# Kernel tuning notes

Hardware: AMD Instinct MI355X
Metric: run time of the kernel (lower is better)

## Reference

```python
import jax, jax.numpy as jnp
import numpy as np
import math

B, S, D, H, DH, R = 2, 2048, 1024, 16, 64, 8
EPS = 1e-5


def setup_inputs() -> dict:
    key = jax.random.key(0)
    ks = jax.random.split(key, 8)
    hidden_states = jax.random.normal(ks[0], (B, S, D), jnp.float32)
    # causal boolean mask (batch, seq, seq); every row has >=1 valid entry
    causal = jnp.tril(jnp.ones((S, S), dtype=bool))
    attention_mask = jnp.broadcast_to(causal, (B, S, S))
    # lora: (n_layers=1, 4, batch, hidden, rank); [0]=qA,[1]=kA,[2]=qB,[3]=kB
    lora = jax.random.normal(ks[1], (1, 4, B, D, R), jnp.float32) * 0.02
    ln_w = jnp.ones((D,), jnp.float32)
    Wq = jax.random.normal(ks[2], (D, D), jnp.float32) * 0.02
    Wk = jax.random.normal(ks[3], (D, D), jnp.float32) * 0.02
    Wv = jax.random.normal(ks[4], (D, D), jnp.float32) * 0.02
    Wo = jax.random.normal(ks[5], (D, D), jnp.float32) * 0.02
    return dict(hidden_states=hidden_states, attention_mask=attention_mask,
                lora=lora, ln_w=ln_w, Wq=Wq, Wk=Wk, Wv=Wv, Wo=Wo)


def _rms_ln(x, w):
    # model_center LayerNorm with bias=False == RMS layernorm
    var = jnp.mean(x * x, axis=-1, keepdims=True)
    return x * jax.lax.rsqrt(var + EPS) * w


def _lora_delta(h, A, Bm):
    # h: (b,s,D), A: (b,D,R), Bm: (b,R,D);  h + (h@A)@Bm * 2
    z = jnp.einsum('bsd,bdr->bsr', h, A)
    return h + jnp.einsum('bsr,brd->bsd', z, Bm) * 2


def reference(hidden_states, attention_mask, lora, ln_w, Wq, Wk, Wv, Wo):
    b, s, _ = hidden_states.shape
    x = _rms_ln(hidden_states, ln_w)
    h_q = x @ Wq.T
    h_k = x @ Wk.T
    h_v = x @ Wv.T
    layer = lora[0]  # (4, b, D, R)
    h_q = _lora_delta(h_q, layer[0], jnp.swapaxes(layer[2], 1, 2))
    h_k = _lora_delta(h_k, layer[1], jnp.swapaxes(layer[3], 1, 2))
    q = h_q.reshape(b, s, H, DH)
    k = h_k.reshape(b, s, H, DH)
    v = h_v.reshape(b, s, H, DH)
    score = jnp.einsum('bqhd,bkhd->bhqk', q, k) / math.sqrt(DH)
    m = attention_mask[:, None, :, :]  # (b,1,s,s)
    score = jnp.where(m, score, -jnp.inf)
    p = jax.nn.softmax(score, axis=-1)
    p = jnp.where(m, p, jnp.float32(0))
    out = jnp.einsum('bhqk,bkhd->bqhd', p, v).reshape(b, s, H * DH)
    out = out @ Wo.T
    return hidden_states + out
```

## Files before the change

kernel.cpp:

```cpp
#include <hip/hip_runtime.h>

typedef __bf16 bf16;
typedef __bf16 bf16x4 __attribute__((ext_vector_type(4)));
typedef __bf16 bf16x8 __attribute__((ext_vector_type(8)));
typedef float f32x4 __attribute__((ext_vector_type(4)));

#define DM 1024
#define NROW 4096
#define SEQ 2048
#define HDIM 64
#define NEGBIG -30000.0f

#define SWB(base, row, bcol) \
  ((char*)(base) + (row) * 128 + ((bcol) ^ (((row) & 7) << 4)))

__device__ __forceinline__ void async16(const bf16* g, bf16* l) {
  __builtin_amdgcn_global_load_lds(
      (const __attribute__((address_space(1))) unsigned int*)g,
      (__attribute__((address_space(3))) unsigned int*)l, 16, 0, 0);
}

template <bool F32OUT>
__device__ __forceinline__ void gemm128(const bf16* __restrict__ A,
                                        const bf16* __restrict__ Bw,
                                        bf16* __restrict__ Cb,
                                        float* __restrict__ Cf,
                                        const float* __restrict__ resid,
                                        int m0, int n0) {
  __shared__ __align__(16) bf16 sA[2][128 * 32];
  __shared__ __align__(16) bf16 sB[2][128 * 32];
  const int t = threadIdx.x;
  const int lane = t & 63;
  const int w = t >> 6;
  const int wm = (w & 1) * 64;
  const int wn = (w >> 1) * 64;
  const int lr = lane & 15;
  const int kg = lane >> 4;

  f32x4 acc[4][4];
#pragma unroll
  for (int i = 0; i < 4; i++)
#pragma unroll
    for (int j = 0; j < 4; j++)
#pragma unroll
      for (int r = 0; r < 4; r++) acc[i][j][r] = 0.0f;

  const int srow = t >> 2;
  const int scol = (t & 3) * 8;
  const bf16* gA = A + (size_t)(m0 + srow) * DM + scol;
  const bf16* gB = Bw + (size_t)(n0 + srow) * DM + scol;

#define GSTAGE(k0_, buf_)                                \
  {                                                      \
    async16(gA + (k0_), &sA[buf_][t * 8]);               \
    async16(gA + (k0_) + 64 * DM, &sA[buf_][t * 8 + 2048]); \
    async16(gB + (k0_), &sB[buf_][t * 8]);               \
    async16(gB + (k0_) + 64 * DM, &sB[buf_][t * 8 + 2048]); \
  }

  GSTAGE(0, 0);
  __syncthreads();

  for (int k0 = 0; k0 < DM; k0 += 32) {
    const int cur = (k0 >> 5) & 1;
    if (k0 + 32 < DM) GSTAGE(k0 + 32, cur ^ 1);
    bf16x8 av[4], bv[4];
#pragma unroll
    for (int mi = 0; mi < 4; mi++)
      av[mi] = *(const bf16x8*)&sA[cur][(wm + mi * 16 + lr) * 32 + kg * 8];
#pragma unroll
    for (int nj = 0; nj < 4; nj++)
      bv[nj] = *(const bf16x8*)&sB[cur][(wn + nj * 16 + lr) * 32 + kg * 8];
    __builtin_amdgcn_s_setprio(1);
#pragma unroll
    for (int mi = 0; mi < 4; mi++)
#pragma unroll
      for (int nj = 0; nj < 4; nj++)
        acc[mi][nj] = __builtin_amdgcn_mfma_f32_16x16x32_bf16(av[mi], bv[nj],
                                                              acc[mi][nj], 0, 0, 0);
    __builtin_amdgcn_s_setprio(0);
    __syncthreads();
  }
#undef GSTAGE

#pragma unroll
  for (int mi = 0; mi < 4; mi++) {
#pragma unroll
    for (int r = 0; r < 4; r++) {
      const int grow = m0 + wm + mi * 16 + kg * 4 + r;
      const size_t base = (size_t)grow * DM + n0 + wn + lr;
#pragma unroll
      for (int nj = 0; nj < 4; nj++) {
        float v = acc[mi][nj][r];
        if (F32OUT) {
          Cf[base + nj * 16] = v + resid[base + nj * 16];
        } else {
          Cb[base + nj * 16] = (bf16)v;
        }
      }
    }
  }
}

__global__ __launch_bounds__(256) void k_pre(const float* __restrict__ hin,
                                             const float* __restrict__ wln,
                                             const float* __restrict__ Wq,
                                             const float* __restrict__ Wk,
                                             const float* __restrict__ Wv,
                                             const float* __restrict__ Wo,
                                             bf16* __restrict__ xo,
                                             bf16* __restrict__ wcast) {
  __shared__ float red[4];
  const int t = threadIdx.x;
  const int bb = blockIdx.x;
  if (bb < NROW) {
    const int row = bb;
    const float4 h4 = ((const float4*)(hin + (size_t)row * DM))[t];
    float ss = h4.x * h4.x + h4.y * h4.y + h4.z * h4.z + h4.w * h4.w;
#pragma unroll
    for (int off = 1; off < 64; off <<= 1) ss += __shfl_xor(ss, off, 64);
    if ((t & 63) == 0) red[t >> 6] = ss;
    __syncthreads();
    ss = red[0] + red[1] + red[2] + red[3];
    const float inv = rsqrtf(ss * (1.0f / DM) + 1e-5f);
    const float4 w4 = ((const float4*)wln)[t];
    bf16x4 o;
    o[0] = (bf16)(h4.x * inv * w4.x);
    o[1] = (bf16)(h4.y * inv * w4.y);
    o[2] = (bf16)(h4.z * inv * w4.z);
    o[3] = (bf16)(h4.w * inv * w4.w);
    *(bf16x4*)&xo[(size_t)row * DM + t * 4] = o;
  } else {
    const int i = (bb - NROW) * 256 + t;
    const int mat = i >> 18;
    const int off = i & 262143;
    const float* s = (mat == 0) ? Wq : (mat == 1) ? Wk : (mat == 2) ? Wv : Wo;
    const float4 v = ((const float4*)s)[off];
    bf16x4 o;
    o[0] = (bf16)v.x; o[1] = (bf16)v.y; o[2] = (bf16)v.z; o[3] = (bf16)v.w;
    ((bf16x4*)wcast)[i] = o;
  }
}

__global__ __launch_bounds__(256) void k_qkv(const bf16* __restrict__ x,
                                             const bf16* __restrict__ Wq,
                                             const bf16* __restrict__ Wk,
                                             const bf16* __restrict__ Wv,
                                             bf16* __restrict__ hq,
                                             bf16* __restrict__ hk,
                                             bf16* __restrict__ hv) {
  const int nb = blockIdx.y;
  const int wsel = nb >> 3;
  const int n0 = (nb & 7) * 128;
  const bf16* Bw = (wsel == 0) ? Wq : (wsel == 1) ? Wk : Wv;
  bf16* C = (wsel == 0) ? hq : (wsel == 1) ? hk : hv;
  gemm128<false>(x, Bw, C, nullptr, nullptr, blockIdx.x * 128, n0);
}

__global__ __launch_bounds__(256) void k_oproj(const bf16* __restrict__ ctx,
                                               const bf16* __restrict__ Wo,
                                               const float* __restrict__ resid,
                                               float* __restrict__ out) {
  gemm128<true>(ctx, Wo, nullptr, out, resid, blockIdx.x * 128, blockIdx.y * 128);
}

__global__ __launch_bounds__(256) void k_mid(const bf16* __restrict__ hv,
                                             bf16* __restrict__ hvT,
                                             bf16* __restrict__ hq,
                                             bf16* __restrict__ hk,
                                             const float* __restrict__ lora) {
  __shared__ __align__(16) char smem[18432];
  const int t = threadIdx.x;
  const int bb = blockIdx.x;
  const int lane = t & 63;
  const int w = t >> 6;
  const int lr = lane & 15;
  const int kg = lane >> 4;

  if (bb < 1024) {
    bf16* sT = (bf16*)smem;
    const int s0 = (bb & 31) * 64;
    const int c0 = ((bb >> 5) & 15) * 64;
    const int b = bb >> 9;
    const int r = t >> 2;
    const int cc = (t & 3) * 16;
    const bf16* g = hv + ((size_t)(b * SEQ + s0 + r)) * DM + c0 + cc;
    const bf16x8 a0 = *(const bf16x8*)g;
    const bf16x8 a1 = *(const bf16x8*)(g + 8);
    *(bf16x8*)SWB(sT, r, cc * 2) = a0;
    *(bf16x8*)SWB(sT, r, cc * 2 + 16) = a1;
    __syncthreads();
    bf16x8 o0, o1;
#pragma unroll
    for (int j = 0; j < 8; j++) {
      o0[j] = *(const bf16*)SWB(sT, cc + j, r * 2);
      o1[j] = *(const bf16*)SWB(sT, cc + 8 + j, r * 2);
    }
    bf16* o = hvT + ((size_t)(b * DM + c0 + r)) * SEQ + s0 + cc;
    *(bf16x8*)o = o0;
    *(bf16x8*)(o + 8) = o1;
  } else {
    bf16* At = (bf16*)smem;
    float* Zp = (float*)(smem + 16384);
    const int lid = bb - 1024;
    const int row0 = (lid & 127) * 32;
    const int which = lid >> 7;
    const int b = row0 >> 11;
    bf16* H = (which == 0 ? hq : hk) + (size_t)row0 * DM;
    const float* Am = lora + (size_t)(which == 0 ? 0 : 1) * 16384 + (size_t)b * 8192;
    const float* Bm = lora + (size_t)(which == 0 ? 2 : 3) * 16384 + (size_t)b * 8192;

    const int d0 = lane * 16;
    float4 Bv[32];
    {
      const float4* bp = (const float4*)(Bm + (size_t)d0 * 8);
#pragma unroll
      for (int i = 0; i < 32; i++) Bv[i] = bp[i];
    }

    {
      const float4* ap = (const float4*)(Am + (size_t)t * 32);
#pragma unroll
      for (int i = 0; i < 8; i++) {
        const float4 v = ap[i];
        const int idx = t * 32 + i * 4;
        At[(idx & 7) * 1024 + (idx >> 3)]             = (bf16)v.x;
        At[((idx + 1) & 7) * 1024 + ((idx + 1) >> 3)] = (bf16)v.y;
        At[((idx + 2) & 7) * 1024 + ((idx + 2) >> 3)] = (bf16)v.z;
        At[((idx + 3) & 7) * 1024 + ((idx + 3) >> 3)] = (bf16)v.w;
      }
    }
    __syncthreads();

    const int tile = w & 1;
    const int khalf = w >> 1;
    {
      f32x4 zacc;
#pragma unroll
      for (int r = 0; r < 4; r++) zacc[r] = 0.f;
      const bf16* gH = H + (size_t)(tile * 16 + lr) * DM + khalf * 512 + kg * 8;
      const bf16* lA = &At[(lr & 7) * 1024 + khalf * 512 + kg * 8];
#pragma unroll
      for (int i = 0; i < 16; i++) {
        const bf16x8 ah = *(const bf16x8*)(gH + i * 32);
        const bf16x8 ba = *(const bf16x8*)(lA + i * 32);
        zacc = __builtin_amdgcn_mfma_f32_16x16x32_bf16(ah, ba, zacc, 0, 0, 0);
      }
      if (lr < 8) {
#pragma unroll
        for (int r = 0; r < 4; r++)
          Zp[(khalf * 32 + tile * 16 + kg * 4 + r) * 8 + lr] = zacc[r];
      }
    }
    __syncthreads();

#pragma unroll
    for (int rr = 0; rr < 8; rr++) {
      const int row = w * 8 + rr;
      const float4 z0 = *(const float4*)&Zp[(row) * 8 + 0];
      const float4 z1 = *(const float4*)&Zp[(row) * 8 + 4];
      const float4 y0 = *(const float4*)&Zp[(32 + row) * 8 + 0];
      const float4 y1 = *(const float4*)&Zp[(32 + row) * 8 + 4];
      const float za = z0.x + y0.x, zb = z0.y + y0.y, zc = z0.z + y0.z, zd = z0.w + y0.w;
      const float ze = z1.x + y1.x, zf = z1.y + y1.y, zg = z1.z + y1.z, zh = z1.w + y1.w;
      bf16* hp = H + (size_t)row * DM + d0;
      const bf16x8 h0 = *(const bf16x8*)hp;
      const bf16x8 h1 = *(const bf16x8*)(hp + 8);
      bf16x8 o0, o1;
#pragma unroll
      for (int j = 0; j < 16; j++) {
        const float4 b0 = Bv[2 * j];
        const float4 b1 = Bv[2 * j + 1];
        const float delta = za * b0.x + zb * b0.y + zc * b0.z + zd * b0.w +
                            ze * b1.x + zf * b1.y + zg * b1.z + zh * b1.w;
        const float hj = (j < 8) ? (float)h0[j] : (float)h1[j - 8];
        const bf16 ov = (bf16)(hj + 2.0f * delta);
        if (j < 8) o0[j] = ov; else o1[j - 8] = ov;
      }
      *(bf16x8*)hp = o0;
      *(bf16x8*)(hp + 8) = o1;
    }
  }
}

__global__ __launch_bounds__(256, 4) void k_attn(const bf16* __restrict__ hq,
                                                 const bf16* __restrict__ hk,
                                                 const bf16* __restrict__ hvT,
                                                 bf16* __restrict__ ctx) {
  const int n = blockIdx.x;
  const int slab = n & 31;
  const int hh = slab & 15;
  const int b = slab >> 4;
  const int xx = n >> 5;
  const int s = xx >> 3;
  const int v = xx & 7;
  const int qt = (s == 0) ? 4 * v : (s == 1) ? 31 - 4 * v
               : (s == 2) ? 4 * v + 2 : 29 - 4 * v;
  const int qbase = qt * 64;

  const int t = threadIdx.x;
  const int lane = t & 63;
  const int w = t >> 6;
  const int lr = lane & 15;
  const int kg = lane >> 4;

  __shared__ __align__(16) bf16 sQ[64 * 64];
  __shared__ __align__(16) bf16 sK[64 * 64];
  __shared__ __align__(16) bf16 sVt[64 * 64];
  __shared__ __align__(16) bf16 sP[64 * 64];

  const size_t rowbase = (size_t)b * SEQ;
  const int hoff = hh * HDIM;
  const float sscale = 0.18033688011112042f;

  const int r4 = t >> 2;
  const int ce = (t & 3) * 16;
  const int cb = (t & 3) * 32;

  {
    const bf16* g = hq + (rowbase + qbase + r4) * DM + hoff + ce;
    bf16x8 q0 = *(const bf16x8*)g;
    bf16x8 q1 = *(const bf16x8*)(g + 8);
    bf16x8 o0, o1;
#pragma unroll
    for (int j = 0; j < 8; j++) {
      o0[j] = (bf16)((float)q0[j] * sscale);
      o1[j] = (bf16)((float)q1[j] * sscale);
    }
    *(bf16x8*)SWB(sQ, r4, cb) = o0;
    *(bf16x8*)SWB(sQ, r4, cb + 16) = o1;
  }

  const bf16* gK = hk + (rowbase + r4) * DM + hoff + ce;
  const bf16* gV = hvT + ((size_t)slab * HDIM + r4) * SEQ + ce;
  bf16x8 kr0 = *(const bf16x8*)gK;
  bf16x8 kr1 = *(const bf16x8*)(gK + 8);
  bf16x8 vr0 = *(const bf16x8*)gV;
  bf16x8 vr1 = *(const bf16x8*)(gV + 8);

  float m_l = NEGBIG, l_l = 0.f;
  f32x4 oacc[4];
#pragma unroll
  for (int nj = 0; nj < 4; nj++)
#pragma unroll
    for (int r = 0; r < 4; r++) oacc[nj][r] = 0.f;

  __syncthreads();

  for (int kt = 0; kt <= qt; kt++) {
    *(bf16x8*)SWB(sK, r4, cb) = kr0;
    *(bf16x8*)SWB(sK, r4, cb + 16) = kr1;
    *(bf16x8*)SWB(sVt, r4, cb) = vr0;
    *(bf16x8*)SWB(sVt, r4, cb + 16) = vr1;
    __syncthreads();

    if (kt < qt) {
      const bf16* gK2 = gK + (size_t)(kt + 1) * 64 * DM;
      const bf16* gV2 = gV + (kt + 1) * 64;
      kr0 = *(const bf16x8*)gK2;
      kr1 = *(const bf16x8*)(gK2 + 8);
      vr0 = *(const bf16x8*)gV2;
      vr1 = *(const bf16x8*)(gV2 + 8);
    }

    f32x4 sc[4];
#pragma unroll
    for (int nj = 0; nj < 4; nj++)
#pragma unroll
      for (int r = 0; r < 4; r++) sc[nj][r] = 0.f;
    __builtin_amdgcn_s_setprio(1);
#pragma unroll
    for (int ks = 0; ks < 2; ks++) {
      const bf16x8 bq = *(const bf16x8*)SWB(sQ, w * 16 + lr, ks * 64 + kg * 16);
#pragma unroll
      for (int nj = 0; nj < 4; nj++) {
        const bf16x8 ak = *(const bf16x8*)SWB(sK, nj * 16 + lr, ks * 64 + kg * 16);
        sc[nj] = __builtin_amdgcn_mfma_f32_16x16x32_bf16(ak, bq, sc[nj], 0, 0, 0);
      }
    }
    __builtin_amdgcn_s_setprio(0);

    if (kt == qt) {
      const int ql = w * 16 + lr;
#pragma unroll
      for (int nj = 0; nj < 4; nj++)
#pragma unroll
        for (int r = 0; r < 4; r++) {
          const int kl = nj * 16 + kg * 4 + r;
          sc[nj][r] = (kl <= ql) ? sc[nj][r] : NEGBIG;
        }
    }

    float rm = sc[0][0];
#pragma unroll
    for (int nj = 0; nj < 4; nj++)
#pragma unroll
      for (int r = 0; r < 4; r++) rm = fmaxf(rm, sc[nj][r]);
    rm = fmaxf(rm, __shfl_xor(rm, 16, 64));
    rm = fmaxf(rm, __shfl_xor(rm, 32, 64));
    const float mnew = fmaxf(m_l, rm);
    const float alpha = __builtin_amdgcn_exp2f(m_l - mnew);
    float rs = 0.f;
#pragma unroll
    for (int nj = 0; nj < 4; nj++)
#pragma unroll
      for (int r = 0; r < 4; r++) {
        const float p = __builtin_amdgcn_exp2f(sc[nj][r] - mnew);
        sc[nj][r] = p;
        rs += p;
      }
    rs += __shfl_xor(rs, 16, 64);
    rs += __shfl_xor(rs, 32, 64);
    l_l = l_l * alpha + rs;
    m_l = mnew;

#pragma unroll
    for (int nj = 0; nj < 4; nj++) {
      bf16x4 p4;
#pragma unroll
      for (int r = 0; r < 4; r++) p4[r] = (bf16)sc[nj][r];
      *(bf16x4*)SWB(sP, w * 16 + lr, nj * 32 + kg * 8) = p4;
    }

#pragma unroll
    for (int r = 0; r < 4; r++) {
      const float ar = __shfl(alpha, (lane & 48) | (kg * 4 + r), 64);
#pragma unroll
      for (int nj = 0; nj < 4; nj++) oacc[nj][r] *= ar;
    }

    __builtin_amdgcn_s_setprio(1);
#pragma unroll
    for (int ks = 0; ks < 2; ks++) {
      const bf16x8 ap = *(const bf16x8*)SWB(sP, w * 16 + lr, ks * 64 + kg * 16);
#pragma unroll
      for (int nj = 0; nj < 4; nj++) {
        const bf16x8 bv = *(const bf16x8*)SWB(sVt, nj * 16 + lr, ks * 64 + kg * 16);
        oacc[nj] = __builtin_amdgcn_mfma_f32_16x16x32_bf16(ap, bv, oacc[nj], 0, 0, 0);
      }
    }
    __builtin_amdgcn_s_setprio(0);
    __syncthreads();
  }

#pragma unroll
  for (int r = 0; r < 4; r++) {
    const float lrow = __shfl(l_l, (lane & 48) | (kg * 4 + r), 64);
    const float invl = 1.0f / lrow;
    const int qr = qbase + w * 16 + kg * 4 + r;
    const size_t base = (rowbase + qr) * DM + hoff + lr;
#pragma unroll
    for (int nj = 0; nj < 4; nj++)
      ctx[base + nj * 16] = (bf16)(oacc[nj][r] * invl);
  }
}

extern "C" void kernel_launch(void* const* d_in, const int* in_sizes, int n_in,
                              void* d_out, int out_size, void* d_ws, size_t ws_size,
                              hipStream_t stream) {
  const float* hidden = (const float*)d_in[0];
  const float* lora = (const float*)d_in[2];
  const float* wln  = (const float*)d_in[3];
  const float* Wq   = (const float*)d_in[4];
  const float* Wk   = (const float*)d_in[5];
  const float* Wv   = (const float*)d_in[6];
  const float* Wo   = (const float*)d_in[7];
  float* out = (float*)d_out;

  const size_t BUF = (size_t)NROW * DM;
  if (ws_size < 4 * BUF * sizeof(bf16)) return;
  bf16* ws = (bf16*)d_ws;
  bf16* hq  = ws;
  bf16* hk  = ws + 1 * BUF;
  bf16* hv  = ws + 2 * BUF;
  bf16* ctx = ws + 3 * BUF;

  bf16* dob = (bf16*)d_out;
  bf16* x   = dob;
  bf16* wqb = dob + BUF;
  bf16* wkb = dob + BUF + DM * DM;
  bf16* wvb = dob + BUF + 2 * DM * DM;
  bf16* wob = dob + BUF + 3 * DM * DM;
  bf16* hvT = dob;

  k_pre<<<dim3(2 * NROW), dim3(256), 0, stream>>>(hidden, wln, Wq, Wk, Wv, Wo, x, wqb);
  k_qkv<<<dim3(32, 24), dim3(256), 0, stream>>>(x, wqb, wkb, wvb, hq, hk, hv);
  k_mid<<<dim3(1280), dim3(256), 0, stream>>>(hv, hvT, hq, hk, lora);
  k_attn<<<dim3(1024), dim3(256), 0, stream>>>(hq, hk, hvT, ctx);
  k_oproj<<<dim3(32, 8), dim3(256), 0, stream>>>(ctx, wob, hidden, out);
}
```

Measured before the change: 219.2 us.

## Enlarge attention query tile to 128 rows with lazy softmax rescaling

The attention kernel now processes 128 query rows per block (32 per wave, two MFMA row groups), so each K/V tile loaded into shared memory is reused across twice as many queries and the grid halves. Causal scheduling pairs query tiles to balance work, and waves whose rows lie entirely above the diagonal skip the final tile. The online-softmax rescale of the accumulators is skipped when the running max grows by at most 8 (in log2 units), which saves multiplies but allows larger intermediate values. Register pressure rises, and launch bounds drop to 3 blocks per SIMD to accommodate it.

Result: no change. 222.2 us (+1.3%).

```diff
diff --git a/kernel.cpp b/kernel.cpp
--- a/kernel.cpp
+++ b/kernel.cpp
@@ -283,7 +283,7 @@
   }
 }
 
-__global__ __launch_bounds__(256, 4) void k_attn(const bf16* __restrict__ hq,
+__global__ __launch_bounds__(256, 3) void k_attn(const bf16* __restrict__ hq,
                                                  const bf16* __restrict__ hk,
                                                  const bf16* __restrict__ hvT,
                                                  bf16* __restrict__ ctx) {
@@ -292,11 +292,9 @@
   const int hh = slab & 15;
   const int b = slab >> 4;
   const int xx = n >> 5;
-  const int s = xx >> 3;
-  const int v = xx & 7;
-  const int qt = (s == 0) ? 4 * v : (s == 1) ? 31 - 4 * v
-               : (s == 2) ? 4 * v + 2 : 29 - 4 * v;
-  const int qbase = qt * 64;
+  const int qt = (xx < 8) ? 2 * xx : 31 - 2 * xx;
+  const int qbase = qt * 128;
+  const int NT = 2 * qt + 2;
 
   const int t = threadIdx.x;
   const int lane = t & 63;
@@ -304,33 +302,32 @@
   const int lr = lane & 15;
   const int kg = lane >> 4;
 
-  __shared__ __align__(16) bf16 sQ[64 * 64];
+  __shared__ __align__(16) bf16 sQ[128 * 64];
   __shared__ __align__(16) bf16 sK[64 * 64];
   __shared__ __align__(16) bf16 sVt[64 * 64];
-  __shared__ __align__(16) bf16 sP[64 * 64];
+  __shared__ __align__(16) bf16 sP[128 * 64];
 
   const size_t rowbase = (size_t)b * SEQ;
   const int hoff = hh * HDIM;
   const float sscale = 0.18033688011112042f;
 
+  {
+    const int r = t >> 1;
+    const int ch = (t & 1) * 32;
+    const bf16* g = hq + (rowbase + qbase + r) * DM + hoff + ch;
+#pragma unroll
+    for (int i = 0; i < 4; i++) {
+      bf16x8 qv = *(const bf16x8*)(g + i * 8);
+      bf16x8 o;
+#pragma unroll
+      for (int j = 0; j < 8; j++) o[j] = (bf16)((float)qv[j] * sscale);
+      *(bf16x8*)SWB(sQ, r, ch * 2 + i * 16) = o;
+    }
+  }
+
   const int r4 = t >> 2;
   const int ce = (t & 3) * 16;
   const int cb = (t & 3) * 32;
-
-  {
-    const bf16* g = hq + (rowbase + qbase + r4) * DM + hoff + ce;
-    bf16x8 q0 = *(const bf16x8*)g;
-    bf16x8 q1 = *(const bf16x8*)(g + 8);
-    bf16x8 o0, o1;
-#pragma unroll
-    for (int j = 0; j < 8; j++) {
-      o0[j] = (bf16)((float)q0[j] * sscale);
-      o1[j] = (bf16)((float)q1[j] * sscale);
-    }
-    *(bf16x8*)SWB(sQ, r4, cb) = o0;
-    *(bf16x8*)SWB(sQ, r4, cb + 16) = o1;
-  }
-
   const bf16* gK = hk + (rowbase + r4) * DM + hoff + ce;
   const bf16* gV = hvT + ((size_t)slab * HDIM + r4) * SEQ + ce;
   bf16x8 kr0 = *(const bf16x8*)gK;
@@ -338,23 +335,25 @@
   bf16x8 vr0 = *(const bf16x8*)gV;
   bf16x8 vr1 = *(const bf16x8*)(gV + 8);
 
-  float m_l = NEGBIG, l_l = 0.f;
-  f32x4 oacc[4];
-#pragma unroll
-  for (int nj = 0; nj < 4; nj++)
-#pragma unroll
-    for (int r = 0; r < 4; r++) oacc[nj][r] = 0.f;
+  float m0 = NEGBIG, m1 = NEGBIG, l0 = 0.f, l1 = 0.f;
+  f32x4 oacc[2][4];
+#pragma unroll
+  for (int qi = 0; qi < 2; qi++)
+#pragma unroll
+    for (int nj = 0; nj < 4; nj++)
+#pragma unroll
+      for (int r = 0; r < 4; r++) oacc[qi][nj][r] = 0.f;
 
   __syncthreads();
 
-  for (int kt = 0; kt <= qt; kt++) {
+  for (int kt = 0; kt < NT; kt++) {
     *(bf16x8*)SWB(sK, r4, cb) = kr0;
     *(bf16x8*)SWB(sK, r4, cb + 16) = kr1;
     *(bf16x8*)SWB(sVt, r4, cb) = vr0;
     *(bf16x8*)SWB(sVt, r4, cb + 16) = vr1;
     __syncthreads();
 
-    if (kt < qt) {
+    if (kt + 1 < NT) {
       const bf16* gK2 = gK + (size_t)(kt + 1) * 64 * DM;
       const bf16* gV2 = gV + (kt + 1) * 64;
       kr0 = *(const bf16x8*)gK2;
@@ -363,95 +362,141 @@
       vr1 = *(const bf16x8*)(gV2 + 8);
     }
 
-    f32x4 sc[4];
-#pragma unroll
-    for (int nj = 0; nj < 4; nj++)
-#pragma unroll
-      for (int r = 0; r < 4; r++) sc[nj][r] = 0.f;
-    __builtin_amdgcn_s_setprio(1);
-#pragma unroll
-    for (int ks = 0; ks < 2; ks++) {
-      const bf16x8 bq = *(const bf16x8*)SWB(sQ, w * 16 + lr, ks * 64 + kg * 16);
-#pragma unroll
-      for (int nj = 0; nj < 4; nj++) {
-        const bf16x8 ak = *(const bf16x8*)SWB(sK, nj * 16 + lr, ks * 64 + kg * 16);
-        sc[nj] = __builtin_amdgcn_mfma_f32_16x16x32_bf16(ak, bq, sc[nj], 0, 0, 0);
-      }
-    }
-    __builtin_amdgcn_s_setprio(0);
-
-    if (kt == qt) {
-      const int ql = w * 16 + lr;
+    const bool act = (w >= 2) || (kt + 1 < NT);
+    if (act) {
+      f32x4 sc[2][4];
+#pragma unroll
+      for (int qi = 0; qi < 2; qi++)
+#pragma unroll
+        for (int nj = 0; nj < 4; nj++)
+#pragma unroll
+          for (int r = 0; r < 4; r++) sc[qi][nj][r] = 0.f;
+
+      __builtin_amdgcn_s_setprio(1);
+#pragma unroll
+      for (int ks = 0; ks < 2; ks++) {
+        bf16x8 ak[4];
+#pragma unroll
+        for (int nj = 0; nj < 4; nj++)
+          ak[nj] = *(const bf16x8*)SWB(sK, nj * 16 + lr, ks * 64 + kg * 16);
+        const bf16x8 bq0 = *(const bf16x8*)SWB(sQ, w * 32 + lr, ks * 64 + kg * 16);
+        const bf16x8 bq1 = *(const bf16x8*)SWB(sQ, w * 32 + 16 + lr, ks * 64 + kg * 16);
+#pragma unroll
+        for (int nj = 0; nj < 4; nj++)
+          sc[0][nj] = __builtin_amdgcn_mfma_f32_16x16x32_bf16(ak[nj], bq0, sc[0][nj], 0, 0, 0);
+#pragma unroll
+        for (int nj = 0; nj < 4; nj++)
+          sc[1][nj] = __builtin_amdgcn_mfma_f32_16x16x32_bf16(ak[nj], bq1, sc[1][nj], 0, 0, 0);
+      }
+      __builtin_amdgcn_s_setprio(0);
+
+      if ((w < 2) ? (kt == NT - 2) : (kt == NT - 1)) {
+        const int kb = kt * 64 + kg * 4;
+        const int qa0 = qbase + w * 32 + lr;
+#pragma unroll
+        for (int qi = 0; qi < 2; qi++) {
+          const int qa = qa0 + qi * 16;
+#pragma unroll
+          for (int nj = 0; nj < 4; nj++)
+#pragma unroll
+            for (int r = 0; r < 4; r++)
+              if (kb + nj * 16 + r > qa) sc[qi][nj][r] = NEGBIG;
+        }
+      }
+
+      float rm0 = sc[0][0][0], rm1 = sc[1][0][0];
 #pragma unroll
       for (int nj = 0; nj < 4; nj++)
 #pragma unroll
         for (int r = 0; r < 4; r++) {
-          const int kl = nj * 16 + kg * 4 + r;
-          sc[nj][r] = (kl <= ql) ? sc[nj][r] : NEGBIG;
+          rm0 = fmaxf(rm0, sc[0][nj][r]);
+          rm1 = fmaxf(rm1, sc[1][nj][r]);
         }
-    }
-
-    float rm = sc[0][0];
-#pragma unroll
-    for (int nj = 0; nj < 4; nj++)
-#pragma unroll
-      for (int r = 0; r < 4; r++) rm = fmaxf(rm, sc[nj][r]);
-    rm = fmaxf(rm, __shfl_xor(rm, 16, 64));
-    rm = fmaxf(rm, __shfl_xor(rm, 32, 64));
-    const float mnew = fmaxf(m_l, rm);
-    const float alpha = __builtin_amdgcn_exp2f(m_l - mnew);
-    float rs = 0.f;
-#pragma unroll
-    for (int nj = 0; nj < 4; nj++)
-#pragma unroll
-      for (int r = 0; r < 4; r++) {
-        const float p = __builtin_amdgcn_exp2f(sc[nj][r] - mnew);
-        sc[nj][r] = p;
-        rs += p;
-      }
-    rs += __shfl_xor(rs, 16, 64);
-    rs += __shfl_xor(rs, 32, 64);
-    l_l = l_l * alpha + rs;
-    m_l = mnew;
-
-#pragma unroll
-    for (int nj = 0; nj < 4; nj++) {
-      bf16x4 p4;
-#pragma unroll
-      for (int r = 0; r < 4; r++) p4[r] = (bf16)sc[nj][r];
-      *(bf16x4*)SWB(sP, w * 16 + lr, nj * 32 + kg * 8) = p4;
-    }
-
+      rm0 = fmaxf(rm0, __shfl_xor(rm0, 16, 64));
+      rm0 = fmaxf(rm0, __shfl_xor(rm0, 32, 64));
+      rm1 = fmaxf(rm1, __shfl_xor(rm1, 16, 64));
+      rm1 = fmaxf(rm1, __shfl_xor(rm1, 32, 64));
+
+      const bool skip = __all((rm0 - m0 <= 8.0f) && (rm1 - m1 <= 8.0f));
+      if (!skip) {
+        const float mn0 = fmaxf(m0, rm0);
+        const float mn1 = fmaxf(m1, rm1);
+        const float a0 = __builtin_amdgcn_exp2f(m0 - mn0);
+        const float a1 = __builtin_amdgcn_exp2f(m1 - mn1);
+        l0 *= a0; l1 *= a1;
+        m0 = mn0; m1 = mn1;
+#pragma unroll
+        for (int r = 0; r < 4; r++) {
+          const float ar0 = __shfl(a0, (lane & 48) | (kg * 4 + r), 64);
+          const float ar1 = __shfl(a1, (lane & 48) | (kg * 4 + r), 64);
+#pragma unroll
+          for (int nj = 0; nj < 4; nj++) {
+            oacc[0][nj][r] *= ar0;
+            oacc[1][nj][r] *= ar1;
+          }
+        }
+      }
+
+      float rs0 = 0.f, rs1 = 0.f;
+#pragma unroll
+      for (int nj = 0; nj < 4; nj++)
+#pragma unroll
+        for (int r = 0; r < 4; r++) {
+          const float p0 = __builtin_amdgcn_exp2f(sc[0][nj][r] - m0);
+          const float p1 = __builtin_amdgcn_exp2f(sc[1][nj][r] - m1);
+          sc[0][nj][r] = p0; rs0 += p0;
+          sc[1][nj][r] = p1; rs1 += p1;
+        }
+      rs0 += __shfl_xor(rs0, 16, 64);
+      rs0 += __shfl_xor(rs0, 32, 64);
+      rs1 += __shfl_xor(rs1, 16, 64);
+      rs1 += __shfl_xor(rs1, 32, 64);
+      l0 += rs0; l1 += rs1;
+
+#pragma unroll
+      for (int qi = 0; qi < 2; qi++)
+#pragma unroll
+        for (int nj = 0; nj < 4; nj++) {
+          bf16x4 p4;
+#pragma unroll
+          for (int r = 0; r < 4; r++) p4[r] = (bf16)sc[qi][nj][r];
+          *(bf16x4*)SWB(sP, w * 32 + qi * 16 + lr, nj * 32 + kg * 8) = p4;
+        }
+
+      __builtin_amdgcn_s_setprio(1);
+#pragma unroll
+      for (int ks = 0; ks < 2; ks++) {
+        bf16x8 bv[4];
+#pragma unroll
+        for (int nj = 0; nj < 4; nj++)
+          bv[nj] = *(const bf16x8*)SWB(sVt, nj * 16 + lr, ks * 64 + kg * 16);
+        const bf16x8 ap0 = *(const bf16x8*)SWB(sP, w * 32 + lr, ks * 64 + kg * 16);
+        const bf16x8 ap1 = *(const bf16x8*)SWB(sP, w * 32 + 16 + lr, ks * 64 + kg * 16);
+#pragma unroll
+        for (int nj = 0; nj < 4; nj++)
+          oacc[0][nj] = __builtin_amdgcn_mfma_f32_16x16x32_bf16(ap0, bv[nj], oacc[0][nj], 0, 0, 0);
+#pragma unroll
+        for (int nj = 0; nj < 4; nj++)
+          oacc[1][nj] = __builtin_amdgcn_mfma_f32_16x16x32_bf16(ap1, bv[nj], oacc[1][nj], 0, 0, 0);
+      }
+      __builtin_amdgcn_s_setprio(0);
+    }
+    __syncthreads();
+  }
+
+#pragma unroll
+  for (int qi = 0; qi < 2; qi++) {
+    const float lq = qi ? l1 : l0;
 #pragma unroll
     for (int r = 0; r < 4; r++) {
-      const float ar = __shfl(alpha, (lane & 48) | (kg * 4 + r), 64);
-#pragma unroll
-      for (int nj = 0; nj < 4; nj++) oacc[nj][r] *= ar;
-    }
-
-    __builtin_amdgcn_s_setprio(1);
-#pragma unroll
-    for (int ks = 0; ks < 2; ks++) {
-      const bf16x8 ap = *(const bf16x8*)SWB(sP, w * 16 + lr, ks * 64 + kg * 16);
-#pragma unroll
-      for (int nj = 0; nj < 4; nj++) {
-        const bf16x8 bv = *(const bf16x8*)SWB(sVt, nj * 16 + lr, ks * 64 + kg * 16);
-        oacc[nj] = __builtin_amdgcn_mfma_f32_16x16x32_bf16(ap, bv, oacc[nj], 0, 0, 0);
-      }
-    }
-    __builtin_amdgcn_s_setprio(0);
-    __syncthreads();
-  }
-
-#pragma unroll
-  for (int r = 0; r < 4; r++) {
-    const float lrow = __shfl(l_l, (lane & 48) | (kg * 4 + r), 64);
-    const float invl = 1.0f / lrow;
-    const int qr = qbase + w * 16 + kg * 4 + r;
-    const size_t base = (rowbase + qr) * DM + hoff + lr;
-#pragma unroll
-    for (int nj = 0; nj < 4; nj++)
-      ctx[base + nj * 16] = (bf16)(oacc[nj][r] * invl);
+      const float lrow = __shfl(lq, (lane & 48) | (kg * 4 + r), 64);
+      const float invl = 1.0f / lrow;
+      const int qr = qbase + w * 32 + qi * 16 + kg * 4 + r;
+      const size_t base = (rowbase + qr) * DM + hoff + lr;
+#pragma unroll
+      for (int nj = 0; nj < 4; nj++)
+        ctx[base + nj * 16] = (bf16)(oacc[qi][nj][r] * invl);
+    }
   }
 }
 
@@ -486,6 +531,6 @@
   k_pre<<<dim3(2 * NROW), dim3(256), 0, stream>>>(hidden, wln, Wq, Wk, Wv, Wo, x, wqb);
   k_qkv<<<dim3(32, 24), dim3(256), 0, stream>>>(x, wqb, wkb, wvb, hq, hk, hv);
   k_mid<<<dim3(1280), dim3(256), 0, stream>>>(hv, hvT, hq, hk, lora);
-  k_attn<<<dim3(1024), dim3(256), 0, stream>>>(hq, hk, hvT, ctx);
+  k_attn<<<dim3(512), dim3(256), 0, stream>>>(hq, hk, hvT, ctx);
   k_oproj<<<dim3(32, 8), dim3(256), 0, stream>>>(ctx, wob, hidden, out);
 }
```
